# Optimization experiments

Measured on AMD Instinct MI355X. Metric: run time of the kernel, lower is better.

Reference implementation:

```python
import jax, jax.numpy as jnp
import numpy as np

N_NODES = 50000
N_EDGES = 800000
D_IN = 128
D_OUT = 128


def setup_inputs() -> dict:
    key = jax.random.key(0)
    k_h, k_w, k_src, k_dst, k_W, k_b = jax.random.split(key, 6)
    h = jax.random.normal(k_h, (N_NODES, D_IN), dtype=jnp.float32)
    w = jax.random.uniform(k_w, (N_EDGES,), dtype=jnp.float32)
    src = jax.random.randint(k_src, (N_EDGES,), 0, N_NODES, dtype=jnp.int32)
    dst = jax.random.randint(k_dst, (N_EDGES,), 0, N_NODES, dtype=jnp.int32)
    W = jax.random.normal(k_W, (D_OUT, D_IN), dtype=jnp.float32) * (1.0 / np.sqrt(D_IN))
    b = jax.random.normal(k_b, (D_OUT,), dtype=jnp.float32) * 0.01
    return {"h": h, "w": w, "src": src, "dst": dst, "W": W, "b": b}


def reference(h, w, src, dst, W, b):
    # u_mul_e: message on each edge = h[src] * w  (scalar edge weight broadcast)
    msg = h[src] * w[:, None]                                   # [E, D_IN]
    # mean aggregation by destination node (DGL fn.mean): sum / in-degree, 0 for isolated nodes
    agg = jax.ops.segment_sum(msg, dst, num_segments=N_NODES)   # [N, D_IN]
    deg = jax.ops.segment_sum(jnp.ones_like(w), dst, num_segments=N_NODES)  # [N]
    h_mean = jnp.where(deg[:, None] > 0, agg / jnp.maximum(deg, 1.0)[:, None], 0.0)
    h_act = jnp.tanh(h_mean)
    return h_act @ W.T + b                                      # [N, D_OUT]
```

## Files before the change

kernel.cpp:

```cpp
#include <hip/hip_runtime.h>
#include <hip/hip_bf16.h>

#define N_NODES 50000
#define N_EDGES 800000
#define D 128
#define NBUCKET 392
#define SLOT 2688
#define PCHUNK 2048
#define NPBLK ((N_EDGES + PCHUNK - 1) / PCHUNK)

typedef __attribute__((ext_vector_type(8))) short bf16x8;
typedef __attribute__((ext_vector_type(4))) float f32x4;

__device__ inline unsigned short f2bf(float f) {
  unsigned u = __float_as_uint(f);
  unsigned r = (u + 0x7FFFu + ((u >> 16) & 1u)) >> 16;
  return (unsigned short)r;
}

__global__ __launch_bounds__(256) void prep_kernel(const float* __restrict__ h,
                                                   unsigned* __restrict__ h8,
                                                   float* __restrict__ scale,
                                                   int* __restrict__ gcursor,
                                                   const float4* __restrict__ Wm4,
                                                   ushort4* __restrict__ W4) {
  int t = threadIdx.x;
  int b = blockIdx.x;
  if (b < 6250) {
    int g = t & 31;
    int node = b * 8 + (t >> 5);
    float4 f = ((const float4*)h)[node * 32 + g];
    float A = fmaxf(fmaxf(fabsf(f.x), fabsf(f.y)), fmaxf(fabsf(f.z), fabsf(f.w)));
#pragma unroll
    for (int off = 16; off >= 1; off >>= 1) A = fmaxf(A, __shfl_xor(A, off, 64));
    float inv = (A > 0.f) ? 127.f / A : 0.f;
    int q0 = (int)rintf(f.x * inv);
    int q1 = (int)rintf(f.y * inv);
    int q2 = (int)rintf(f.z * inv);
    int q3 = (int)rintf(f.w * inv);
    h8[node * 32 + g] = (unsigned)(q0 & 0xFF) | ((unsigned)(q1 & 0xFF) << 8) |
                        ((unsigned)(q2 & 0xFF) << 16) | ((unsigned)(q3 & 0xFF) << 24);
    if (g == 0) scale[node] = A / (127.f * 511.f);
  } else if (b < 6266) {
    int i = (b - 6250) * 256 + t;
    float4 f = Wm4[i];
    ushort4 o;
    o.x = f2bf(f.x); o.y = f2bf(f.y); o.z = f2bf(f.z); o.w = f2bf(f.w);
    W4[i] = o;
  } else {
    if (t < NBUCKET) gcursor[t] = t * SLOT;
    int t2 = t + 256;
    if (t2 < NBUCKET) gcursor[t2] = t2 * SLOT;
  }
}

__global__ __launch_bounds__(256) void partition_kernel(const int* __restrict__ src,
                                                        const int* __restrict__ dst,
                                                        const float* __restrict__ w,
                                                        int* __restrict__ gcursor,
                                                        unsigned* __restrict__ csr4) {
  __shared__ int lhist[NBUCKET];
  __shared__ int lstart[NBUCKET];
  __shared__ int lcur[NBUCKET];
  __shared__ int gbase[NBUCKET];
  __shared__ unsigned staged_v[PCHUNK];
  __shared__ unsigned short staged_b[PCHUNK];
  int t = threadIdx.x;
  int e0 = blockIdx.x * PCHUNK;
  int nch = N_EDGES - e0; if (nch > PCHUNK) nch = PCHUNK;

  for (int i = t; i < NBUCKET; i += 256) lhist[i] = 0;
  __syncthreads();

  unsigned rec[PCHUNK / 256];
  int rbkt[PCHUNK / 256];
#pragma unroll
  for (int k = 0; k < PCHUNK / 256; ++k) {
    int idx = t + k * 256;
    if (idx < nch) {
      int e = e0 + idx;
      int s = src[e];
      int d_ = dst[e];
      unsigned q = (unsigned)__float2uint_rn(w[e] * 511.f);
      rbkt[k] = d_ >> 7;
      rec[k] = ((unsigned)s << 16) | ((unsigned)(d_ & 127) << 9) | q;
      atomicAdd(&lhist[rbkt[k]], 1);
    } else {
      rbkt[k] = -1;
      rec[k] = 0;
    }
  }
  __syncthreads();

  if (t < 64) {
    int carry = 0;
    for (int base = 0; base < NBUCKET; base += 64) {
      int i = base + t;
      int v = (i < NBUCKET) ? lhist[i] : 0;
      int incl = v;
#pragma unroll
      for (int off = 1; off < 64; off <<= 1) {
        int y = __shfl_up(incl, off, 64);
        if (t >= off) incl += y;
      }
      if (i < NBUCKET) lstart[i] = incl - v + carry;
      carry += __shfl(incl, 63, 64);
    }
  }
  __syncthreads();

  for (int i = t; i < NBUCKET; i += 256) {
    gbase[i] = (lhist[i] > 0) ? atomicAdd(&gcursor[i], lhist[i]) : 0;
    lcur[i] = lstart[i];
  }
  __syncthreads();

#pragma unroll
  for (int k = 0; k < PCHUNK / 256; ++k) {
    if (rbkt[k] >= 0) {
      int lp = atomicAdd(&lcur[rbkt[k]], 1);
      staged_v[lp] = rec[k];
      staged_b[lp] = (unsigned short)rbkt[k];
    }
  }
  __syncthreads();

  for (int i = t; i < nch; i += 256) {
    int bkt = staged_b[i];
    csr4[gbase[bkt] + (i - lstart[bkt])] = staged_v[i];
  }
}

__global__ __launch_bounds__(256) void scatter2_kernel(const unsigned* __restrict__ csr4,
                                                       const int* __restrict__ gcursor,
                                                       int* __restrict__ row_start,
                                                       unsigned* __restrict__ csr_ew) {
  __shared__ int cnt[128];
  __shared__ int base[128];
  int b = blockIdx.x, t = threadIdx.x;
  if (t < 128) cnt[t] = 0;
  __syncthreads();
  int base0 = b * SLOT;
  int end = gcursor[b];
  for (int i = base0 + t; i < end; i += 256)
    atomicAdd(&cnt[(csr4[i] >> 9) & 127], 1);
  __syncthreads();
  if (t < 64) {
    int carry = base0;
    for (int c = 0; c < 2; ++c) {
      int v = cnt[c * 64 + t];
      int incl = v;
#pragma unroll
      for (int off = 1; off < 64; off <<= 1) {
        int y = __shfl_up(incl, off, 64);
        if (t >= off) incl += y;
      }
      base[c * 64 + t] = incl - v + carry;
      carry += __shfl(incl, 63, 64);
    }
  }
  __syncthreads();
  if (t < 128) { row_start[b * 129 + t] = base[t]; cnt[t] = base[t]; }
  if (t == 0) row_start[b * 129 + 128] = end;
  __syncthreads();
  for (int i = base0 + t; i < end; i += 256) {
    unsigned v = csr4[i];
    int pos = atomicAdd(&cnt[(v >> 9) & 127], 1);
    csr_ew[pos] = v;
  }
}

__global__ __launch_bounds__(256) void agg_gemm_kernel(const uint2* __restrict__ h8,
                                                       const float* __restrict__ scale,
                                                       const unsigned* __restrict__ csr_ew,
                                                       const int* __restrict__ row_start,
                                                       const unsigned short* __restrict__ W_bf,
                                                       const float* __restrict__ bias,
                                                       float* __restrict__ out) {
  __shared__ unsigned short hact[16][136];
  int t = threadIdx.x;
  int lane = t & 63, wid = t >> 6;
  int q = lane >> 4, c = lane & 15;
  int n0 = blockIdx.x * 16;

#pragma unroll
  for (int i = 0; i < 4; ++i) {
    int node = n0 + wid * 4 + i;
    int rsb = (node >> 7) * 129 + (node & 127);
    int beg = row_start[rsb], end = row_start[rsb + 1];
    float a[8] = {0.f, 0.f, 0.f, 0.f, 0.f, 0.f, 0.f, 0.f};
    int e = beg + q;
    for (; e + 12 < end; e += 16) {
      unsigned p0 = csr_ew[e],      p1 = csr_ew[e + 4];
      unsigned p2 = csr_ew[e + 8],  p3 = csr_ew[e + 12];
      int s0 = p0 >> 16, s1 = p1 >> 16, s2 = p2 >> 16, s3 = p3 >> 16;
      uint2 v0 = h8[s0 * 16 + c];
      uint2 v1 = h8[s1 * 16 + c];
      uint2 v2 = h8[s2 * 16 + c];
      uint2 v3 = h8[s3 * 16 + c];
      float m0 = scale[s0] * (float)(p0 & 0x1FFu);
      float m1 = scale[s1] * (float)(p1 & 0x1FFu);
      float m2 = scale[s2] * (float)(p2 & 0x1FFu);
      float m3 = scale[s3] * (float)(p3 & 0x1FFu);
#pragma unroll
      for (int j = 0; j < 2; ++j) {
        unsigned w0 = (&v0.x)[j], w1 = (&v1.x)[j], w2 = (&v2.x)[j], w3 = (&v3.x)[j];
        a[4*j+0] = fmaf((float)(signed char)(w0 & 0xFF), m0, a[4*j+0]);
        a[4*j+1] = fmaf((float)(signed char)((w0 >> 8) & 0xFF), m0, a[4*j+1]);
        a[4*j+2] = fmaf((float)(signed char)((w0 >> 16) & 0xFF), m0, a[4*j+2]);
        a[4*j+3] = fmaf((float)(signed char)(w0 >> 24), m0, a[4*j+3]);
        a[4*j+0] = fmaf((float)(signed char)(w1 & 0xFF), m1, a[4*j+0]);
        a[4*j+1] = fmaf((float)(signed char)((w1 >> 8) & 0xFF), m1, a[4*j+1]);
        a[4*j+2] = fmaf((float)(signed char)((w1 >> 16) & 0xFF), m1, a[4*j+2]);
        a[4*j+3] = fmaf((float)(signed char)(w1 >> 24), m1, a[4*j+3]);
        a[4*j+0] = fmaf((float)(signed char)(w2 & 0xFF), m2, a[4*j+0]);
        a[4*j+1] = fmaf((float)(signed char)((w2 >> 8) & 0xFF), m2, a[4*j+1]);
        a[4*j+2] = fmaf((float)(signed char)((w2 >> 16) & 0xFF), m2, a[4*j+2]);
        a[4*j+3] = fmaf((float)(signed char)(w2 >> 24), m2, a[4*j+3]);
        a[4*j+0] = fmaf((float)(signed char)(w3 & 0xFF), m3, a[4*j+0]);
        a[4*j+1] = fmaf((float)(signed char)((w3 >> 8) & 0xFF), m3, a[4*j+1]);
        a[4*j+2] = fmaf((float)(signed char)((w3 >> 16) & 0xFF), m3, a[4*j+2]);
        a[4*j+3] = fmaf((float)(signed char)(w3 >> 24), m3, a[4*j+3]);
      }
    }
    for (; e + 4 < end; e += 8) {
      unsigned p0 = csr_ew[e], p1 = csr_ew[e + 4];
      int s0 = p0 >> 16, s1 = p1 >> 16;
      uint2 v0 = h8[s0 * 16 + c];
      uint2 v1 = h8[s1 * 16 + c];
      float m0 = scale[s0] * (float)(p0 & 0x1FFu);
      float m1 = scale[s1] * (float)(p1 & 0x1FFu);
#pragma unroll
      for (int j = 0; j < 2; ++j) {
        unsigned w0 = (&v0.x)[j], w1 = (&v1.x)[j];
        a[4*j+0] = fmaf((float)(signed char)(w0 & 0xFF), m0, a[4*j+0]);
        a[4*j+1] = fmaf((float)(signed char)((w0 >> 8) & 0xFF), m0, a[4*j+1]);
        a[4*j+2] = fmaf((float)(signed char)((w0 >> 16) & 0xFF), m0, a[4*j+2]);
        a[4*j+3] = fmaf((float)(signed char)(w0 >> 24), m0, a[4*j+3]);
        a[4*j+0] = fmaf((float)(signed char)(w1 & 0xFF), m1, a[4*j+0]);
        a[4*j+1] = fmaf((float)(signed char)((w1 >> 8) & 0xFF), m1, a[4*j+1]);
        a[4*j+2] = fmaf((float)(signed char)((w1 >> 16) & 0xFF), m1, a[4*j+2]);
        a[4*j+3] = fmaf((float)(signed char)(w1 >> 24), m1, a[4*j+3]);
      }
    }
    if (e < end) {
      unsigned p = csr_ew[e];
      int s = p >> 16;
      uint2 v = h8[s * 16 + c];
      float m = scale[s] * (float)(p & 0x1FFu);
#pragma unroll
      for (int j = 0; j < 2; ++j) {
        unsigned wv = (&v.x)[j];
        a[4*j+0] = fmaf((float)(signed char)(wv & 0xFF), m, a[4*j+0]);
        a[4*j+1] = fmaf((float)(signed char)((wv >> 8) & 0xFF), m, a[4*j+1]);
        a[4*j+2] = fmaf((float)(signed char)((wv >> 16) & 0xFF), m, a[4*j+2]);
        a[4*j+3] = fmaf((float)(signed char)(wv >> 24), m, a[4*j+3]);
      }
    }
#pragma unroll
    for (int k = 0; k < 8; ++k) {
      a[k] += __shfl_xor(a[k], 16, 64);
      a[k] += __shfl_xor(a[k], 32, 64);
    }
    int deg = end - beg;
    float inv = (deg > 0) ? 1.f / (float)deg : 0.f;
    float t0 = tanhf(a[2 * q] * inv);
    float t1 = tanhf(a[2 * q + 1] * inv);
    unsigned r = (unsigned)f2bf(t0) | ((unsigned)f2bf(t1) << 16);
    *(unsigned*)&hact[wid * 4 + i][c * 8 + q * 2] = r;
  }
  __syncthreads();

  int m = lane & 15;
  int kg = lane >> 4;
  bf16x8 afrag[4];
#pragma unroll
  for (int kc = 0; kc < 4; ++kc)
    afrag[kc] = *(const bf16x8*)&hact[m][kc * 32 + kg * 8];

#pragma unroll
  for (int jj = 0; jj < 2; ++jj) {
    int jt = wid * 2 + jj;
    int j = jt * 16 + m;
    const unsigned short* wrow = W_bf + j * D;
    f32x4 acc = {0.f, 0.f, 0.f, 0.f};
#pragma unroll
    for (int kc = 0; kc < 4; ++kc) {
      bf16x8 bb = *(const bf16x8*)(wrow + kc * 32 + kg * 8);
      acc = __builtin_amdgcn_mfma_f32_16x16x32_bf16(afrag[kc], bb, acc, 0, 0, 0);
    }
    float bj = bias[j];
#pragma unroll
    for (int rr = 0; rr < 4; ++rr) {
      int nn = n0 + kg * 4 + rr;
      out[(size_t)nn * D + j] = acc[rr] + bj;
    }
  }
}

extern "C" void kernel_launch(void* const* d_in, const int* in_sizes, int n_in,
                              void* d_out, int out_size, void* d_ws, size_t ws_size,
                              hipStream_t stream) {
  const float* h    = (const float*)d_in[0];
  const float* w    = (const float*)d_in[1];
  const int*   src  = (const int*)d_in[2];
  const int*   dst  = (const int*)d_in[3];
  const float* Wm   = (const float*)d_in[4];
  const float* bias = (const float*)d_in[5];
  float* out = (float*)d_out;

  char* ws = (char*)d_ws;
  int*            gcursor   = (int*)(ws);
  unsigned short* W_bf      = (unsigned short*)(ws + 1600);
  float*          scale     = (float*)(ws + 34368);
  unsigned*       h8        = (unsigned*)(ws + 234368);
  int*            row_start = (int*)(ws + 6634368);
  unsigned*       csr4      = (unsigned*)(ws + 6836640);
  unsigned*       csr_ew    = (unsigned*)(ws + 11051424);

  prep_kernel<<<6267, 256, 0, stream>>>(h, h8, scale, gcursor, (const float4*)Wm, (ushort4*)W_bf);
  partition_kernel<<<NPBLK, 256, 0, stream>>>(src, dst, w, gcursor, csr4);
  scatter2_kernel<<<391, 256, 0, stream>>>(csr4, gcursor, row_start, csr_ew);
  agg_gemm_kernel<<<N_NODES / 16, 256, 0, stream>>>((const uint2*)h8, scale, csr_ew,
                                                    row_start, W_bf, bias, out);
}
```

Baseline: 75.52 us.

## Split int8 feature table into two column halves and gather each in separate passes

The quantized node feature table is stored as two half-width tables (first and second 64 features), and the aggregation kernel runs two passes, each gathering 4-byte rows from one half. The aim is a smaller working set per pass so the gathered table fits better in cache. In exchange, edge indices and scales are read twice and the per-lane 8-byte gather becomes two 4-byte gathers. It also swaps tanhf and the division for a fast exp/rcp-based approximation, which slightly reduces accuracy.

```diff
diff --git a/kernel.cpp b/kernel.cpp
--- a/kernel.cpp
+++ b/kernel.cpp
@@ -18,8 +18,14 @@
   return (unsigned short)r;
 }
 
+__device__ inline float fast_tanh(float x) {
+  float g = __expf(2.0f * x);
+  return 1.0f - 2.0f * __builtin_amdgcn_rcpf(g + 1.0f);
+}
+
 __global__ __launch_bounds__(256) void prep_kernel(const float* __restrict__ h,
-                                                   unsigned* __restrict__ h8,
+                                                   unsigned* __restrict__ h8a,
+                                                   unsigned* __restrict__ h8b,
                                                    float* __restrict__ scale,
                                                    int* __restrict__ gcursor,
                                                    const float4* __restrict__ Wm4,
@@ -38,8 +44,10 @@
     int q1 = (int)rintf(f.y * inv);
     int q2 = (int)rintf(f.z * inv);
     int q3 = (int)rintf(f.w * inv);
-    h8[node * 32 + g] = (unsigned)(q0 & 0xFF) | ((unsigned)(q1 & 0xFF) << 8) |
-                        ((unsigned)(q2 & 0xFF) << 16) | ((unsigned)(q3 & 0xFF) << 24);
+    unsigned val = (unsigned)(q0 & 0xFF) | ((unsigned)(q1 & 0xFF) << 8) |
+                   ((unsigned)(q2 & 0xFF) << 16) | ((unsigned)(q3 & 0xFF) << 24);
+    if (g < 16) h8a[node * 16 + g] = val;
+    else        h8b[node * 16 + (g - 16)] = val;
     if (g == 0) scale[node] = A / (127.f * 511.f);
   } else if (b < 6266) {
     int i = (b - 6250) * 256 + t;
@@ -170,7 +178,8 @@
   }
 }
 
-__global__ __launch_bounds__(256) void agg_gemm_kernel(const uint2* __restrict__ h8,
+__global__ __launch_bounds__(256) void agg_gemm_kernel(const unsigned* __restrict__ h8a,
+                                                       const unsigned* __restrict__ h8b,
                                                        const float* __restrict__ scale,
                                                        const unsigned* __restrict__ csr_ew,
                                                        const int* __restrict__ row_start,
@@ -183,91 +192,88 @@
   int q = lane >> 4, c = lane & 15;
   int n0 = blockIdx.x * 16;
 
+  int begs[4], ends[4];
 #pragma unroll
   for (int i = 0; i < 4; ++i) {
     int node = n0 + wid * 4 + i;
     int rsb = (node >> 7) * 129 + (node & 127);
-    int beg = row_start[rsb], end = row_start[rsb + 1];
-    float a[8] = {0.f, 0.f, 0.f, 0.f, 0.f, 0.f, 0.f, 0.f};
-    int e = beg + q;
-    for (; e + 12 < end; e += 16) {
-      unsigned p0 = csr_ew[e],      p1 = csr_ew[e + 4];
-      unsigned p2 = csr_ew[e + 8],  p3 = csr_ew[e + 12];
-      int s0 = p0 >> 16, s1 = p1 >> 16, s2 = p2 >> 16, s3 = p3 >> 16;
-      uint2 v0 = h8[s0 * 16 + c];
-      uint2 v1 = h8[s1 * 16 + c];
-      uint2 v2 = h8[s2 * 16 + c];
-      uint2 v3 = h8[s3 * 16 + c];
-      float m0 = scale[s0] * (float)(p0 & 0x1FFu);
-      float m1 = scale[s1] * (float)(p1 & 0x1FFu);
-      float m2 = scale[s2] * (float)(p2 & 0x1FFu);
-      float m3 = scale[s3] * (float)(p3 & 0x1FFu);
-#pragma unroll
-      for (int j = 0; j < 2; ++j) {
-        unsigned w0 = (&v0.x)[j], w1 = (&v1.x)[j], w2 = (&v2.x)[j], w3 = (&v3.x)[j];
-        a[4*j+0] = fmaf((float)(signed char)(w0 & 0xFF), m0, a[4*j+0]);
-        a[4*j+1] = fmaf((float)(signed char)((w0 >> 8) & 0xFF), m0, a[4*j+1]);
-        a[4*j+2] = fmaf((float)(signed char)((w0 >> 16) & 0xFF), m0, a[4*j+2]);
-        a[4*j+3] = fmaf((float)(signed char)(w0 >> 24), m0, a[4*j+3]);
-        a[4*j+0] = fmaf((float)(signed char)(w1 & 0xFF), m1, a[4*j+0]);
-        a[4*j+1] = fmaf((float)(signed char)((w1 >> 8) & 0xFF), m1, a[4*j+1]);
-        a[4*j+2] = fmaf((float)(signed char)((w1 >> 16) & 0xFF), m1, a[4*j+2]);
-        a[4*j+3] = fmaf((float)(signed char)(w1 >> 24), m1, a[4*j+3]);
-        a[4*j+0] = fmaf((float)(signed char)(w2 & 0xFF), m2, a[4*j+0]);
-        a[4*j+1] = fmaf((float)(signed char)((w2 >> 8) & 0xFF), m2, a[4*j+1]);
-        a[4*j+2] = fmaf((float)(signed char)((w2 >> 16) & 0xFF), m2, a[4*j+2]);
-        a[4*j+3] = fmaf((float)(signed char)(w2 >> 24), m2, a[4*j+3]);
-        a[4*j+0] = fmaf((float)(signed char)(w3 & 0xFF), m3, a[4*j+0]);
-        a[4*j+1] = fmaf((float)(signed char)((w3 >> 8) & 0xFF), m3, a[4*j+1]);
-        a[4*j+2] = fmaf((float)(signed char)((w3 >> 16) & 0xFF), m3, a[4*j+2]);
-        a[4*j+3] = fmaf((float)(signed char)(w3 >> 24), m3, a[4*j+3]);
-      }
-    }
-    for (; e + 4 < end; e += 8) {
-      unsigned p0 = csr_ew[e], p1 = csr_ew[e + 4];
-      int s0 = p0 >> 16, s1 = p1 >> 16;
-      uint2 v0 = h8[s0 * 16 + c];
-      uint2 v1 = h8[s1 * 16 + c];
-      float m0 = scale[s0] * (float)(p0 & 0x1FFu);
-      float m1 = scale[s1] * (float)(p1 & 0x1FFu);
-#pragma unroll
-      for (int j = 0; j < 2; ++j) {
-        unsigned w0 = (&v0.x)[j], w1 = (&v1.x)[j];
-        a[4*j+0] = fmaf((float)(signed char)(w0 & 0xFF), m0, a[4*j+0]);
-        a[4*j+1] = fmaf((float)(signed char)((w0 >> 8) & 0xFF), m0, a[4*j+1]);
-        a[4*j+2] = fmaf((float)(signed char)((w0 >> 16) & 0xFF), m0, a[4*j+2]);
-        a[4*j+3] = fmaf((float)(signed char)(w0 >> 24), m0, a[4*j+3]);
-        a[4*j+0] = fmaf((float)(signed char)(w1 & 0xFF), m1, a[4*j+0]);
-        a[4*j+1] = fmaf((float)(signed char)((w1 >> 8) & 0xFF), m1, a[4*j+1]);
-        a[4*j+2] = fmaf((float)(signed char)((w1 >> 16) & 0xFF), m1, a[4*j+2]);
-        a[4*j+3] = fmaf((float)(signed char)(w1 >> 24), m1, a[4*j+3]);
-      }
-    }
-    if (e < end) {
-      unsigned p = csr_ew[e];
-      int s = p >> 16;
-      uint2 v = h8[s * 16 + c];
-      float m = scale[s] * (float)(p & 0x1FFu);
-#pragma unroll
-      for (int j = 0; j < 2; ++j) {
-        unsigned wv = (&v.x)[j];
-        a[4*j+0] = fmaf((float)(signed char)(wv & 0xFF), m, a[4*j+0]);
-        a[4*j+1] = fmaf((float)(signed char)((wv >> 8) & 0xFF), m, a[4*j+1]);
-        a[4*j+2] = fmaf((float)(signed char)((wv >> 16) & 0xFF), m, a[4*j+2]);
-        a[4*j+3] = fmaf((float)(signed char)(wv >> 24), m, a[4*j+3]);
-      }
-    }
-#pragma unroll
-    for (int k = 0; k < 8; ++k) {
-      a[k] += __shfl_xor(a[k], 16, 64);
-      a[k] += __shfl_xor(a[k], 32, 64);
-    }
-    int deg = end - beg;
-    float inv = (deg > 0) ? 1.f / (float)deg : 0.f;
-    float t0 = tanhf(a[2 * q] * inv);
-    float t1 = tanhf(a[2 * q + 1] * inv);
-    unsigned r = (unsigned)f2bf(t0) | ((unsigned)f2bf(t1) << 16);
-    *(unsigned*)&hact[wid * 4 + i][c * 8 + q * 2] = r;
+    begs[i] = row_start[rsb];
+    ends[i] = row_start[rsb + 1];
+  }
+
+#pragma unroll
+  for (int p = 0; p < 2; ++p) {
+    const unsigned* __restrict__ tab = p ? h8b : h8a;
+#pragma unroll
+    for (int i = 0; i < 4; ++i) {
+      int end = ends[i];
+      float a0 = 0.f, a1 = 0.f, a2 = 0.f, a3 = 0.f;
+      int e = begs[i] + q;
+      for (; e + 12 < end; e += 16) {
+        unsigned p0 = csr_ew[e],      p1 = csr_ew[e + 4];
+        unsigned p2 = csr_ew[e + 8],  p3 = csr_ew[e + 12];
+        int s0 = p0 >> 16, s1 = p1 >> 16, s2 = p2 >> 16, s3 = p3 >> 16;
+        unsigned v0 = tab[s0 * 16 + c];
+        unsigned v1 = tab[s1 * 16 + c];
+        unsigned v2 = tab[s2 * 16 + c];
+        unsigned v3 = tab[s3 * 16 + c];
+        float m0 = scale[s0] * (float)(p0 & 0x1FFu);
+        float m1 = scale[s1] * (float)(p1 & 0x1FFu);
+        float m2 = scale[s2] * (float)(p2 & 0x1FFu);
+        float m3 = scale[s3] * (float)(p3 & 0x1FFu);
+        a0 = fmaf((float)(signed char)(v0 & 0xFF), m0, a0);
+        a1 = fmaf((float)(signed char)((v0 >> 8) & 0xFF), m0, a1);
+        a2 = fmaf((float)(signed char)((v0 >> 16) & 0xFF), m0, a2);
+        a3 = fmaf((float)(signed char)(v0 >> 24), m0, a3);
+        a0 = fmaf((float)(signed char)(v1 & 0xFF), m1, a0);
+        a1 = fmaf((float)(signed char)((v1 >> 8) & 0xFF), m1, a1);
+        a2 = fmaf((float)(signed char)((v1 >> 16) & 0xFF), m1, a2);
+        a3 = fmaf((float)(signed char)(v1 >> 24), m1, a3);
+        a0 = fmaf((float)(signed char)(v2 & 0xFF), m2, a0);
+        a1 = fmaf((float)(signed char)((v2 >> 8) & 0xFF), m2, a1);
+        a2 = fmaf((float)(signed char)((v2 >> 16) & 0xFF), m2, a2);
+        a3 = fmaf((float)(signed char)(v2 >> 24), m2, a3);
+        a0 = fmaf((float)(signed char)(v3 & 0xFF), m3, a0);
+        a1 = fmaf((float)(signed char)((v3 >> 8) & 0xFF), m3, a1);
+        a2 = fmaf((float)(signed char)((v3 >> 16) & 0xFF), m3, a2);
+        a3 = fmaf((float)(signed char)(v3 >> 24), m3, a3);
+      }
+      for (; e + 4 < end; e += 8) {
+        unsigned p0 = csr_ew[e], p1 = csr_ew[e + 4];
+        int s0 = p0 >> 16, s1 = p1 >> 16;
+        unsigned v0 = tab[s0 * 16 + c];
+        unsigned v1 = tab[s1 * 16 + c];
+        float m0 = scale[s0] * (float)(p0 & 0x1FFu);
+        float m1 = scale[s1] * (float)(p1 & 0x1FFu);
+        a0 = fmaf((float)(signed char)(v0 & 0xFF), m0, a0);
+        a1 = fmaf((float)(signed char)((v0 >> 8) & 0xFF), m0, a1);
+        a2 = fmaf((float)(signed char)((v0 >> 16) & 0xFF), m0, a2);
+        a3 = fmaf((float)(signed char)(v0 >> 24), m0, a3);
+        a0 = fmaf((float)(signed char)(v1 & 0xFF), m1, a0);
+        a1 = fmaf((float)(signed char)((v1 >> 8) & 0xFF), m1, a1);
+        a2 = fmaf((float)(signed char)((v1 >> 16) & 0xFF), m1, a2);
+        a3 = fmaf((float)(signed char)(v1 >> 24), m1, a3);
+      }
+      if (e < end) {
+        unsigned p0 = csr_ew[e];
+        int s0 = p0 >> 16;
+        unsigned v0 = tab[s0 * 16 + c];
+        float m0 = scale[s0] * (float)(p0 & 0x1FFu);
+        a0 = fmaf((float)(signed char)(v0 & 0xFF), m0, a0);
+        a1 = fmaf((float)(signed char)((v0 >> 8) & 0xFF), m0, a1);
+        a2 = fmaf((float)(signed char)((v0 >> 16) & 0xFF), m0, a2);
+        a3 = fmaf((float)(signed char)(v0 >> 24), m0, a3);
+      }
+      a0 += __shfl_xor(a0, 16, 64); a0 += __shfl_xor(a0, 32, 64);
+      a1 += __shfl_xor(a1, 16, 64); a1 += __shfl_xor(a1, 32, 64);
+      a2 += __shfl_xor(a2, 16, 64); a2 += __shfl_xor(a2, 32, 64);
+      a3 += __shfl_xor(a3, 16, 64); a3 += __shfl_xor(a3, 32, 64);
+      int deg = end - begs[i];
+      float inv = (deg > 0) ? __builtin_amdgcn_rcpf((float)deg) : 0.f;
+      float sel = (q == 0) ? a0 : (q == 1) ? a1 : (q == 2) ? a2 : a3;
+      float tt = fast_tanh(sel * inv);
+      hact[wid * 4 + i][p * 64 + c * 4 + q] = f2bf(tt);
+    }
   }
   __syncthreads();
 
@@ -313,14 +319,16 @@
   int*            gcursor   = (int*)(ws);
   unsigned short* W_bf      = (unsigned short*)(ws + 1600);
   float*          scale     = (float*)(ws + 34368);
-  unsigned*       h8        = (unsigned*)(ws + 234368);
+  unsigned*       h8a       = (unsigned*)(ws + 234368);
+  unsigned*       h8b       = (unsigned*)(ws + 3434368);
   int*            row_start = (int*)(ws + 6634368);
   unsigned*       csr4      = (unsigned*)(ws + 6836640);
   unsigned*       csr_ew    = (unsigned*)(ws + 11051424);
 
-  prep_kernel<<<6267, 256, 0, stream>>>(h, h8, scale, gcursor, (const float4*)Wm, (ushort4*)W_bf);
+  prep_kernel<<<6267, 256, 0, stream>>>(h, h8a, h8b, scale, gcursor,
+                                        (const float4*)Wm, (ushort4*)W_bf);
   partition_kernel<<<NPBLK, 256, 0, stream>>>(src, dst, w, gcursor, csr4);
   scatter2_kernel<<<391, 256, 0, stream>>>(csr4, gcursor, row_start, csr_ew);
-  agg_gemm_kernel<<<N_NODES / 16, 256, 0, stream>>>((const uint2*)h8, scale, csr_ew,
+  agg_gemm_kernel<<<N_NODES / 16, 256, 0, stream>>>(h8a, h8b, scale, csr_ew,
                                                     row_start, W_bf, bias, out);
 }
```

New measurement: 83.24 us. 1.1x slower.

## Fold per-node scale into 16-bit edge multiplier and use fast tanh

Applied to the files above, without the earlier changes.

The per-source-node dequantization scale is now multiplied into the edge weight during partitioning and stored as a 16-bit fixed-point value in the packed edge record. The aggregation kernel no longer does a random gather of scale[src] per edge. To free the bits, the within-bucket destination index moves to a separate byte array, which scatter2 reads. Also swaps tanhf and the degree division for exp/rcp approximations. The costs are an extra byte stream, a scale gather moved into partition, and precision limits from clamping at 65535.

```diff
diff --git a/kernel.cpp b/kernel.cpp
--- a/kernel.cpp
+++ b/kernel.cpp
@@ -8,6 +8,8 @@
 #define SLOT 2688
 #define PCHUNK 2048
 #define NPBLK ((N_EDGES + PCHUNK - 1) / PCHUNK)
+#define M_ENC 1310700.0f
+#define M_DEC 7.629511e-7f
 
 typedef __attribute__((ext_vector_type(8))) short bf16x8;
 typedef __attribute__((ext_vector_type(4))) float f32x4;
@@ -18,9 +20,14 @@
   return (unsigned short)r;
 }
 
+__device__ inline float fast_tanh(float x) {
+  float g = __expf(2.0f * x);
+  return 1.0f - 2.0f * __builtin_amdgcn_rcpf(g + 1.0f);
+}
+
 __global__ __launch_bounds__(256) void prep_kernel(const float* __restrict__ h,
                                                    unsigned* __restrict__ h8,
-                                                   float* __restrict__ scale,
+                                                   float* __restrict__ scale2,
                                                    int* __restrict__ gcursor,
                                                    const float4* __restrict__ Wm4,
                                                    ushort4* __restrict__ W4) {
@@ -40,7 +47,7 @@
     int q3 = (int)rintf(f.w * inv);
     h8[node * 32 + g] = (unsigned)(q0 & 0xFF) | ((unsigned)(q1 & 0xFF) << 8) |
                         ((unsigned)(q2 & 0xFF) << 16) | ((unsigned)(q3 & 0xFF) << 24);
-    if (g == 0) scale[node] = A / (127.f * 511.f);
+    if (g == 0) scale2[node] = A * (1.0f / 127.0f);
   } else if (b < 6266) {
     int i = (b - 6250) * 256 + t;
     float4 f = Wm4[i];
@@ -57,14 +64,17 @@
 __global__ __launch_bounds__(256) void partition_kernel(const int* __restrict__ src,
                                                         const int* __restrict__ dst,
                                                         const float* __restrict__ w,
+                                                        const float* __restrict__ scale2,
                                                         int* __restrict__ gcursor,
-                                                        unsigned* __restrict__ csr4) {
+                                                        unsigned* __restrict__ csr4,
+                                                        unsigned char* __restrict__ nl8) {
   __shared__ int lhist[NBUCKET];
   __shared__ int lstart[NBUCKET];
   __shared__ int lcur[NBUCKET];
   __shared__ int gbase[NBUCKET];
   __shared__ unsigned staged_v[PCHUNK];
   __shared__ unsigned short staged_b[PCHUNK];
+  __shared__ unsigned char staged_n[PCHUNK];
   int t = threadIdx.x;
   int e0 = blockIdx.x * PCHUNK;
   int nch = N_EDGES - e0; if (nch > PCHUNK) nch = PCHUNK;
@@ -74,6 +84,7 @@
 
   unsigned rec[PCHUNK / 256];
   int rbkt[PCHUNK / 256];
+  int rnl[PCHUNK / 256];
 #pragma unroll
   for (int k = 0; k < PCHUNK / 256; ++k) {
     int idx = t + k * 256;
@@ -81,12 +92,15 @@
       int e = e0 + idx;
       int s = src[e];
       int d_ = dst[e];
-      unsigned q = (unsigned)__float2uint_rn(w[e] * 511.f);
+      float m = scale2[s] * w[e];
+      unsigned q = (unsigned)__float2uint_rn(fminf(m * M_ENC, 65535.0f));
       rbkt[k] = d_ >> 7;
-      rec[k] = ((unsigned)s << 16) | ((unsigned)(d_ & 127) << 9) | q;
+      rnl[k] = d_ & 127;
+      rec[k] = ((unsigned)s << 16) | q;
       atomicAdd(&lhist[rbkt[k]], 1);
     } else {
       rbkt[k] = -1;
+      rnl[k] = 0;
       rec[k] = 0;
     }
   }
@@ -121,17 +135,21 @@
       int lp = atomicAdd(&lcur[rbkt[k]], 1);
       staged_v[lp] = rec[k];
       staged_b[lp] = (unsigned short)rbkt[k];
+      staged_n[lp] = (unsigned char)rnl[k];
     }
   }
   __syncthreads();
 
   for (int i = t; i < nch; i += 256) {
     int bkt = staged_b[i];
-    csr4[gbase[bkt] + (i - lstart[bkt])] = staged_v[i];
+    int pos = gbase[bkt] + (i - lstart[bkt]);
+    csr4[pos] = staged_v[i];
+    nl8[pos] = staged_n[i];
   }
 }
 
 __global__ __launch_bounds__(256) void scatter2_kernel(const unsigned* __restrict__ csr4,
+                                                       const unsigned char* __restrict__ nl8,
                                                        const int* __restrict__ gcursor,
                                                        int* __restrict__ row_start,
                                                        unsigned* __restrict__ csr_ew) {
@@ -143,7 +161,7 @@
   int base0 = b * SLOT;
   int end = gcursor[b];
   for (int i = base0 + t; i < end; i += 256)
-    atomicAdd(&cnt[(csr4[i] >> 9) & 127], 1);
+    atomicAdd(&cnt[nl8[i]], 1);
   __syncthreads();
   if (t < 64) {
     int carry = base0;
@@ -164,14 +182,12 @@
   if (t == 0) row_start[b * 129 + 128] = end;
   __syncthreads();
   for (int i = base0 + t; i < end; i += 256) {
-    unsigned v = csr4[i];
-    int pos = atomicAdd(&cnt[(v >> 9) & 127], 1);
-    csr_ew[pos] = v;
+    int pos = atomicAdd(&cnt[nl8[i]], 1);
+    csr_ew[pos] = csr4[i];
   }
 }
 
 __global__ __launch_bounds__(256) void agg_gemm_kernel(const uint2* __restrict__ h8,
-                                                       const float* __restrict__ scale,
                                                        const unsigned* __restrict__ csr_ew,
                                                        const int* __restrict__ row_start,
                                                        const unsigned short* __restrict__ W_bf,
@@ -198,10 +214,10 @@
       uint2 v1 = h8[s1 * 16 + c];
       uint2 v2 = h8[s2 * 16 + c];
       uint2 v3 = h8[s3 * 16 + c];
-      float m0 = scale[s0] * (float)(p0 & 0x1FFu);
-      float m1 = scale[s1] * (float)(p1 & 0x1FFu);
-      float m2 = scale[s2] * (float)(p2 & 0x1FFu);
-      float m3 = scale[s3] * (float)(p3 & 0x1FFu);
+      float m0 = (float)(p0 & 0xFFFFu) * M_DEC;
+      float m1 = (float)(p1 & 0xFFFFu) * M_DEC;
+      float m2 = (float)(p2 & 0xFFFFu) * M_DEC;
+      float m3 = (float)(p3 & 0xFFFFu) * M_DEC;
 #pragma unroll
       for (int j = 0; j < 2; ++j) {
         unsigned w0 = (&v0.x)[j], w1 = (&v1.x)[j], w2 = (&v2.x)[j], w3 = (&v3.x)[j];
@@ -228,8 +244,8 @@
       int s0 = p0 >> 16, s1 = p1 >> 16;
       uint2 v0 = h8[s0 * 16 + c];
       uint2 v1 = h8[s1 * 16 + c];
-      float m0 = scale[s0] * (float)(p0 & 0x1FFu);
-      float m1 = scale[s1] * (float)(p1 & 0x1FFu);
+      float m0 = (float)(p0 & 0xFFFFu) * M_DEC;
+      float m1 = (float)(p1 & 0xFFFFu) * M_DEC;
 #pragma unroll
       for (int j = 0; j < 2; ++j) {
         unsigned w0 = (&v0.x)[j], w1 = (&v1.x)[j];
@@ -247,7 +263,7 @@
       unsigned p = csr_ew[e];
       int s = p >> 16;
       uint2 v = h8[s * 16 + c];
-      float m = scale[s] * (float)(p & 0x1FFu);
+      float m = (float)(p & 0xFFFFu) * M_DEC;
 #pragma unroll
       for (int j = 0; j < 2; ++j) {
         unsigned wv = (&v.x)[j];
@@ -263,9 +279,9 @@
       a[k] += __shfl_xor(a[k], 32, 64);
     }
     int deg = end - beg;
-    float inv = (deg > 0) ? 1.f / (float)deg : 0.f;
-    float t0 = tanhf(a[2 * q] * inv);
-    float t1 = tanhf(a[2 * q + 1] * inv);
+    float inv = (deg > 0) ? __builtin_amdgcn_rcpf((float)deg) : 0.f;
+    float t0 = fast_tanh(a[2 * q] * inv);
+    float t1 = fast_tanh(a[2 * q + 1] * inv);
     unsigned r = (unsigned)f2bf(t0) | ((unsigned)f2bf(t1) << 16);
     *(unsigned*)&hact[wid * 4 + i][c * 8 + q * 2] = r;
   }
@@ -312,15 +328,17 @@
   char* ws = (char*)d_ws;
   int*            gcursor   = (int*)(ws);
   unsigned short* W_bf      = (unsigned short*)(ws + 1600);
-  float*          scale     = (float*)(ws + 34368);
+  float*          scale2    = (float*)(ws + 34368);
   unsigned*       h8        = (unsigned*)(ws + 234368);
   int*            row_start = (int*)(ws + 6634368);
   unsigned*       csr4      = (unsigned*)(ws + 6836640);
   unsigned*       csr_ew    = (unsigned*)(ws + 11051424);
-
-  prep_kernel<<<6267, 256, 0, stream>>>(h, h8, scale, gcursor, (const float4*)Wm, (ushort4*)W_bf);
-  partition_kernel<<<NPBLK, 256, 0, stream>>>(src, dst, w, gcursor, csr4);
-  scatter2_kernel<<<391, 256, 0, stream>>>(csr4, gcursor, row_start, csr_ew);
-  agg_gemm_kernel<<<N_NODES / 16, 256, 0, stream>>>((const uint2*)h8, scale, csr_ew,
+  unsigned char*  nl8       = (unsigned char*)(ws + 15266208);
+
+  prep_kernel<<<6267, 256, 0, stream>>>(h, h8, scale2, gcursor,
+                                        (const float4*)Wm, (ushort4*)W_bf);
+  partition_kernel<<<NPBLK, 256, 0, stream>>>(src, dst, w, scale2, gcursor, csr4, nl8);
+  scatter2_kernel<<<391, 256, 0, stream>>>(csr4, nl8, gcursor, row_start, csr_ew);
+  agg_gemm_kernel<<<N_NODES / 16, 256, 0, stream>>>((const uint2*)h8, csr_ew,
                                                     row_start, W_bf, bias, out);
 }
```

Result: slower. 77.65 us (+2.8%).

## Fuse quantize prep into partition kernel and use fast tanh/rcp

Applied to the files above, without the earlier changes.

Merges the h int8 quantization and W bf16 conversion blocks into the edge partition kernel as extra blocks, so both run in a single launch and can overlap. The bucket cursors become zero-based offsets cleared by a memset instead of being set inside the prep kernel, which is what removes the ordering dependency between the two. Also replaces tanhf and the division by degree with an exp/rcp-based fast tanh and a hardware reciprocal in the aggregation epilogue. The cost is an extra memset launch, a large kernel whose blocks carry the partition kernel's shared-memory footprint even when they only quantize, and slightly lower precision in the activation.

```diff
diff --git a/kernel.cpp b/kernel.cpp
--- a/kernel.cpp
+++ b/kernel.cpp
@@ -18,47 +18,18 @@
   return (unsigned short)r;
 }
 
-__global__ __launch_bounds__(256) void prep_kernel(const float* __restrict__ h,
-                                                   unsigned* __restrict__ h8,
-                                                   float* __restrict__ scale,
-                                                   int* __restrict__ gcursor,
-                                                   const float4* __restrict__ Wm4,
-                                                   ushort4* __restrict__ W4) {
-  int t = threadIdx.x;
-  int b = blockIdx.x;
-  if (b < 6250) {
-    int g = t & 31;
-    int node = b * 8 + (t >> 5);
-    float4 f = ((const float4*)h)[node * 32 + g];
-    float A = fmaxf(fmaxf(fabsf(f.x), fabsf(f.y)), fmaxf(fabsf(f.z), fabsf(f.w)));
-#pragma unroll
-    for (int off = 16; off >= 1; off >>= 1) A = fmaxf(A, __shfl_xor(A, off, 64));
-    float inv = (A > 0.f) ? 127.f / A : 0.f;
-    int q0 = (int)rintf(f.x * inv);
-    int q1 = (int)rintf(f.y * inv);
-    int q2 = (int)rintf(f.z * inv);
-    int q3 = (int)rintf(f.w * inv);
-    h8[node * 32 + g] = (unsigned)(q0 & 0xFF) | ((unsigned)(q1 & 0xFF) << 8) |
-                        ((unsigned)(q2 & 0xFF) << 16) | ((unsigned)(q3 & 0xFF) << 24);
-    if (g == 0) scale[node] = A / (127.f * 511.f);
-  } else if (b < 6266) {
-    int i = (b - 6250) * 256 + t;
-    float4 f = Wm4[i];
-    ushort4 o;
-    o.x = f2bf(f.x); o.y = f2bf(f.y); o.z = f2bf(f.z); o.w = f2bf(f.w);
-    W4[i] = o;
-  } else {
-    if (t < NBUCKET) gcursor[t] = t * SLOT;
-    int t2 = t + 256;
-    if (t2 < NBUCKET) gcursor[t2] = t2 * SLOT;
-  }
-}
-
-__global__ __launch_bounds__(256) void partition_kernel(const int* __restrict__ src,
-                                                        const int* __restrict__ dst,
-                                                        const float* __restrict__ w,
-                                                        int* __restrict__ gcursor,
-                                                        unsigned* __restrict__ csr4) {
+__device__ inline float fast_tanh(float x) {
+  float g = __expf(2.0f * x);
+  return 1.0f - 2.0f * __builtin_amdgcn_rcpf(g + 1.0f);
+}
+
+__global__ __launch_bounds__(256) void prep_partition_kernel(
+    const float* __restrict__ h, unsigned* __restrict__ h8,
+    float* __restrict__ scale, const float4* __restrict__ Wm4,
+    ushort4* __restrict__ W4,
+    const int* __restrict__ src, const int* __restrict__ dst,
+    const float* __restrict__ w, int* __restrict__ goff,
+    unsigned* __restrict__ csr4) {
   __shared__ int lhist[NBUCKET];
   __shared__ int lstart[NBUCKET];
   __shared__ int lcur[NBUCKET];
@@ -66,7 +37,36 @@
   __shared__ unsigned staged_v[PCHUNK];
   __shared__ unsigned short staged_b[PCHUNK];
   int t = threadIdx.x;
-  int e0 = blockIdx.x * PCHUNK;
+  int b = blockIdx.x;
+
+  if (b >= NPBLK) {
+    int pb = b - NPBLK;
+    if (pb < 6250) {
+      int g = t & 31;
+      int node = pb * 8 + (t >> 5);
+      float4 f = ((const float4*)h)[node * 32 + g];
+      float A = fmaxf(fmaxf(fabsf(f.x), fabsf(f.y)), fmaxf(fabsf(f.z), fabsf(f.w)));
+#pragma unroll
+      for (int off = 16; off >= 1; off >>= 1) A = fmaxf(A, __shfl_xor(A, off, 64));
+      float inv = (A > 0.f) ? 127.f / A : 0.f;
+      int q0 = (int)rintf(f.x * inv);
+      int q1 = (int)rintf(f.y * inv);
+      int q2 = (int)rintf(f.z * inv);
+      int q3 = (int)rintf(f.w * inv);
+      h8[node * 32 + g] = (unsigned)(q0 & 0xFF) | ((unsigned)(q1 & 0xFF) << 8) |
+                          ((unsigned)(q2 & 0xFF) << 16) | ((unsigned)(q3 & 0xFF) << 24);
+      if (g == 0) scale[node] = A / (127.f * 511.f);
+    } else {
+      int i = (pb - 6250) * 256 + t;
+      float4 f = Wm4[i];
+      ushort4 o;
+      o.x = f2bf(f.x); o.y = f2bf(f.y); o.z = f2bf(f.z); o.w = f2bf(f.w);
+      W4[i] = o;
+    }
+    return;
+  }
+
+  int e0 = b * PCHUNK;
   int nch = N_EDGES - e0; if (nch > PCHUNK) nch = PCHUNK;
 
   for (int i = t; i < NBUCKET; i += 256) lhist[i] = 0;
@@ -110,7 +110,7 @@
   __syncthreads();
 
   for (int i = t; i < NBUCKET; i += 256) {
-    gbase[i] = (lhist[i] > 0) ? atomicAdd(&gcursor[i], lhist[i]) : 0;
+    gbase[i] = (lhist[i] > 0) ? (i * SLOT + atomicAdd(&goff[i], lhist[i])) : 0;
     lcur[i] = lstart[i];
   }
   __syncthreads();
@@ -132,7 +132,7 @@
 }
 
 __global__ __launch_bounds__(256) void scatter2_kernel(const unsigned* __restrict__ csr4,
-                                                       const int* __restrict__ gcursor,
+                                                       const int* __restrict__ goff,
                                                        int* __restrict__ row_start,
                                                        unsigned* __restrict__ csr_ew) {
   __shared__ int cnt[128];
@@ -141,7 +141,7 @@
   if (t < 128) cnt[t] = 0;
   __syncthreads();
   int base0 = b * SLOT;
-  int end = gcursor[b];
+  int end = base0 + goff[b];
   for (int i = base0 + t; i < end; i += 256)
     atomicAdd(&cnt[(csr4[i] >> 9) & 127], 1);
   __syncthreads();
@@ -263,9 +263,9 @@
       a[k] += __shfl_xor(a[k], 32, 64);
     }
     int deg = end - beg;
-    float inv = (deg > 0) ? 1.f / (float)deg : 0.f;
-    float t0 = tanhf(a[2 * q] * inv);
-    float t1 = tanhf(a[2 * q + 1] * inv);
+    float inv = (deg > 0) ? __builtin_amdgcn_rcpf((float)deg) : 0.f;
+    float t0 = fast_tanh(a[2 * q] * inv);
+    float t1 = fast_tanh(a[2 * q + 1] * inv);
     unsigned r = (unsigned)f2bf(t0) | ((unsigned)f2bf(t1) << 16);
     *(unsigned*)&hact[wid * 4 + i][c * 8 + q * 2] = r;
   }
@@ -310,7 +310,7 @@
   float* out = (float*)d_out;
 
   char* ws = (char*)d_ws;
-  int*            gcursor   = (int*)(ws);
+  int*            goff      = (int*)(ws);
   unsigned short* W_bf      = (unsigned short*)(ws + 1600);
   float*          scale     = (float*)(ws + 34368);
   unsigned*       h8        = (unsigned*)(ws + 234368);
@@ -318,9 +318,10 @@
   unsigned*       csr4      = (unsigned*)(ws + 6836640);
   unsigned*       csr_ew    = (unsigned*)(ws + 11051424);
 
-  prep_kernel<<<6267, 256, 0, stream>>>(h, h8, scale, gcursor, (const float4*)Wm, (ushort4*)W_bf);
-  partition_kernel<<<NPBLK, 256, 0, stream>>>(src, dst, w, gcursor, csr4);
-  scatter2_kernel<<<391, 256, 0, stream>>>(csr4, gcursor, row_start, csr_ew);
+  hipMemsetAsync(goff, 0, NBUCKET * sizeof(int), stream);
+  prep_partition_kernel<<<NPBLK + 6266, 256, 0, stream>>>(
+      h, h8, scale, (const float4*)Wm, (ushort4*)W_bf, src, dst, w, goff, csr4);
+  scatter2_kernel<<<391, 256, 0, stream>>>(csr4, goff, row_start, csr_ew);
   agg_gemm_kernel<<<N_NODES / 16, 256, 0, stream>>>((const uint2*)h8, scale, csr_ew,
                                                     row_start, W_bf, bias, out);
 }
```

Result: faster. 73.85 us (-2.2%).
